# Performance work log

Measured on AMD Instinct MI355X. Metric: run time of the kernel, lower is better.

## Reference

```python
import jax, jax.numpy as jnp
import numpy as np

V, E, T, H, NT, B = 30000, 300, 256, 256, 9, 128


def setup_inputs() -> dict:
    key = jax.random.key(0)
    ks = jax.random.split(key, 12)
    s = 0.05
    # token ids with trailing zero padding (0 = pad), lens in [T//2, T]
    lens = jax.random.randint(ks[0], (B,), T // 2, T + 1)
    tokens = jax.random.randint(ks[1], (B, T), 1, V)
    pos = jnp.arange(T)[None, :]
    inputs = jnp.where(pos < lens[:, None], tokens, 0)
    labels = jax.random.randint(ks[2], (B, T), 0, NT)
    emb = jax.random.normal(ks[3], (V, E), jnp.float32) * s
    Wf = jax.random.normal(ks[4], (E, 4 * H), jnp.float32) * s
    Uf = jax.random.normal(ks[5], (H, 4 * H), jnp.float32) * s
    bf = jnp.zeros((4 * H,), jnp.float32)
    Wb = jax.random.normal(ks[6], (E, 4 * H), jnp.float32) * s
    Ub = jax.random.normal(ks[7], (H, 4 * H), jnp.float32) * s
    bb = jnp.zeros((4 * H,), jnp.float32)
    fcW = jax.random.normal(ks[8], (2 * H, NT), jnp.float32) * s
    fcb = jnp.zeros((NT,), jnp.float32)
    trans = jax.random.uniform(ks[9], (NT, NT), jnp.float32)  # tf.random.uniform init
    return dict(inputs=inputs, labels=labels, emb=emb, Wf=Wf, Uf=Uf, bf=bf,
                Wb=Wb, Ub=Ub, bb=bb, fcW=fcW, fcb=fcb, trans=trans)


def _lstm(x, W, U, b):
    """Keras LSTM (gate order i,f,g,o). x: [B,T,E] -> [B,T,H]."""
    xW = jnp.einsum('bte,eh->bth', x, W) + b  # precompute input projections

    def step(carry, xt):
        h, c = carry
        z = xt + h @ U
        i, f, g, o = jnp.split(z, 4, axis=-1)
        i = jax.nn.sigmoid(i)
        f = jax.nn.sigmoid(f)
        g = jnp.tanh(g)
        o = jax.nn.sigmoid(o)
        c = f * c + i * g
        h = o * jnp.tanh(c)
        return (h, c), h

    Bq = x.shape[0]
    Hq = U.shape[0]
    init = (jnp.zeros((Bq, Hq), x.dtype), jnp.zeros((Bq, Hq), x.dtype))
    _, hs = jax.lax.scan(step, init, jnp.swapaxes(xW, 0, 1))  # [T,B,H]
    return jnp.swapaxes(hs, 0, 1)


def _crf_log_likelihood(logits, labels, lens, trans):
    """tfa.text.crf_log_likelihood: gold score - log partition. logits: [B,T,N]."""
    Bq, Tq, Nq = logits.shape
    pos = jnp.arange(Tq)[None, :]
    mask = pos < lens[:, None]  # [B,T]
    # unary (emission) score of the gold path
    unary = jnp.take_along_axis(logits, labels[..., None], axis=-1)[..., 0]
    score = jnp.sum(jnp.where(mask, unary, 0.0), axis=-1)
    # binary (transition) score of the gold path
    btrans = trans[labels[:, :-1], labels[:, 1:]]
    bmask = pos[:, 1:] < lens[:, None]
    score = score + jnp.sum(jnp.where(bmask, btrans, 0.0), axis=-1)
    # forward algorithm (log partition) with per-timestep length masking
    def step(alpha, inp):
        logit_t, m_t = inp  # [B,N], [B]
        new = jax.nn.logsumexp(alpha[:, :, None] + trans[None], axis=1) + logit_t
        return jnp.where(m_t[:, None], new, alpha), None

    alpha0 = logits[:, 0]
    xs = (jnp.swapaxes(logits[:, 1:], 0, 1), jnp.swapaxes(mask[:, 1:], 0, 1))
    alpha, _ = jax.lax.scan(step, alpha0, xs)
    log_norm = jax.nn.logsumexp(alpha, axis=-1)
    return score - log_norm


def reference(inputs, labels, emb, Wf, Uf, bf, Wb, Ub, bb, fcW, fcb, trans):
    text_lens = jnp.sum((inputs != 0).astype(jnp.int32), axis=-1)
    x = emb[inputs]  # [B,T,E]
    hf = _lstm(x, Wf, Uf, bf)
    hb = _lstm(x[:, ::-1], Wb, Ub, bb)[:, ::-1]
    h = jnp.concatenate([hf, hb], axis=-1)  # [B,T,2H]
    logits = h @ fcW + fcb  # [B,T,NT]
    log_likelihood = _crf_log_likelihood(logits, labels, text_lens, trans)
    return logits, log_likelihood, text_lens
```

## Files before the change

kernel.cpp:

```cpp
#include <hip/hip_runtime.h>
#include <hip/hip_bf16.h>
#include <stdint.h>

#define Bb 128
#define Tt 256
#define Ee 300
#define EP 320
#define Hh 256
#define G4 1024
#define NTAG 9

typedef __bf16 bf16x8 __attribute__((ext_vector_type(8)));
typedef float f32x4 __attribute__((ext_vector_type(4)));
typedef float f32x2 __attribute__((ext_vector_type(2)));
typedef int i32x8 __attribute__((ext_vector_type(8)));
typedef unsigned short u16;
typedef unsigned int u32;
typedef unsigned char u8;
typedef long i64;

union U4B { uint4 q; bf16x8 v; };

static __device__ __forceinline__ float bf2f(u32 u){
  union { float f; u32 u; } w; w.u = u << 16; return w.f;
}
static __device__ __forceinline__ u16 f2bf(float f){
  union { float f; u32 u; } w; w.f = f;
  u32 x = w.u;
  return (u16)((x + 0x7fffu + ((x >> 16) & 1u)) >> 16);
}
static __device__ __forceinline__ int perm2orig(int c){
  int w = c >> 7, r = c & 127, g = r >> 5, jj = r & 31;
  return g * 256 + w * 32 + jj;
}
static __device__ __forceinline__ float frcp(float x){ return __builtin_amdgcn_rcpf(x); }
static __device__ __forceinline__ float fexp2(float x){
  float r; asm("v_exp_f32 %0, %1" : "=v"(r) : "v"(x)); return r;
}
static __device__ __forceinline__ f32x2 vexp2(f32x2 x){
  f32x2 r; r[0] = fexp2(x[0]); r[1] = fexp2(x[1]); return r;
}
static __device__ __forceinline__ f32x2 vrcp(f32x2 x){
  f32x2 r; r[0] = frcp(x[0]); r[1] = frcp(x[1]); return r;
}
static __device__ __forceinline__ f32x2 vfabs(f32x2 x){
  f32x2 r; r[0] = __builtin_fabsf(x[0]); r[1] = __builtin_fabsf(x[1]); return r;
}
static __device__ __forceinline__ f32x2 vminc(f32x2 x, float c){
  f32x2 r; r[0] = fminf(x[0], c); r[1] = fminf(x[1], c); return r;
}
static __device__ __forceinline__ f32x2 vcps(f32x2 m, f32x2 s){
  f32x2 r; r[0] = __builtin_copysignf(m[0], s[0]);
  r[1] = __builtin_copysignf(m[1], s[1]); return r;
}
static __device__ __forceinline__ void gl_lds16(const void* g, void* l){
  __builtin_amdgcn_global_load_lds((const __attribute__((address_space(1))) u32*)(g),
                                   (__attribute__((address_space(3))) u32*)(l), 16, 0, 0);
}

__global__ void prep_k(const float* __restrict__ Wf, const float* __restrict__ Wb,
                       const float* __restrict__ Uf, const float* __restrict__ Ub,
                       const float* __restrict__ bf_, const float* __restrict__ bb_,
                       const float* __restrict__ fcW,
                       u16* __restrict__ Wpk, u8* __restrict__ Upk8,
                       float* __restrict__ bperm, u8* __restrict__ fcw8){
  int blk = blockIdx.x;
  if(blk < 320){
    int idx = blk * 256 + threadIdx.x;
    if(idx >= 128 * 10 * 64) return;
    int lane = idx & 63;
    int kk = (idx >> 6) % 10;
    int nt2 = idx / 640;
    int d = nt2 >> 6, ntd = nt2 & 63;
    int oc = perm2orig(ntd * 16 + (lane & 15));
    const float* W = d ? Wb : Wf;
    int k0 = kk * 32 + ((lane >> 4) << 3);
    u16 o[8];
    #pragma unroll
    for(int j = 0; j < 8; ++j){
      int k = k0 + j;
      o[j] = (k < Ee) ? f2bf(W[(size_t)k * G4 + oc]) : (u16)0;
    }
    uint4 q;
    q.x = o[0] | ((u32)o[1] << 16); q.y = o[2] | ((u32)o[3] << 16);
    q.z = o[4] | ((u32)o[5] << 16); q.w = o[6] | ((u32)o[7] << 16);
    *(uint4*)(Wpk + (size_t)idx * 8) = q;
  } else if(blk < 384){
    int idx = (blk - 320) * 256 + threadIdx.x;
    if(idx >= 2 * 64 * 2 * 64) return;
    int lane = idx & 63;
    int kh = (idx >> 6) & 1;
    int nt = (idx >> 7) & 63;
    int d = idx >> 13;
    int oc = perm2orig(nt * 16 + (lane & 15));
    const float* U = d ? Ub : Uf;
    int k0 = kh * 128 + (lane >> 4) * 32;
    u32 o[8];
    #pragma unroll
    for(int m = 0; m < 8; ++m){
      float v0 = U[(size_t)(k0 + 4 * m + 0) * G4 + oc] * 32.f;
      float v1 = U[(size_t)(k0 + 4 * m + 1) * G4 + oc] * 32.f;
      float v2 = U[(size_t)(k0 + 4 * m + 2) * G4 + oc] * 32.f;
      float v3 = U[(size_t)(k0 + 4 * m + 3) * G4 + oc] * 32.f;
      int pk = __builtin_amdgcn_cvt_pk_fp8_f32(v0, v1, 0, false);
      pk = __builtin_amdgcn_cvt_pk_fp8_f32(v2, v3, pk, true);
      o[m] = (u32)pk;
    }
    uint4* dst = (uint4*)(Upk8 + (size_t)idx * 32);
    dst[0] = (uint4){o[0], o[1], o[2], o[3]};
    dst[1] = (uint4){o[4], o[5], o[6], o[7]};
  } else if(blk < 392){
    int c = (blk - 384) * 256 + threadIdx.x;
    if(c >= 2048) return;
    const float* src = (c >> 10) ? bb_ : bf_;
    bperm[c] = src[perm2orig(c & 1023)];
  } else {
    int idx = (blk - 392) * 256 + threadIdx.x;
    if(idx >= 1024) return;
    int lane = idx & 63, kk = idx >> 6;
    int col = lane & 15;
    int k0 = kk * 32 + ((lane >> 4) << 3);
    float v[8];
    #pragma unroll
    for(int j = 0; j < 8; ++j)
      v[j] = (col < NTAG) ? fcW[(size_t)(k0 + j) * NTAG + col] * 256.f : 0.f;
    int lo = __builtin_amdgcn_cvt_pk_fp8_f32(v[0], v[1], 0, false);
    lo = __builtin_amdgcn_cvt_pk_fp8_f32(v[2], v[3], lo, true);
    int hi = __builtin_amdgcn_cvt_pk_fp8_f32(v[4], v[5], 0, false);
    hi = __builtin_amdgcn_cvt_pk_fp8_f32(v[6], v[7], hi, true);
    uint2 q; q.x = (u32)lo; q.y = (u32)hi;
    *(uint2*)(fcw8 + (size_t)idx * 8) = q;
  }
}

__global__ void gather_x_k(const int* __restrict__ inp, const float* __restrict__ emb,
                           u16* __restrict__ xbf){
  int row = blockIdx.x * 2 + (threadIdx.x >> 7);
  int j = threadIdx.x & 127;
  int t = row >> 7, b = row & 127;
  int tok = inp[b * Tt + t];
  u16* dst = xbf + (size_t)row * EP;
  if(j < 75){
    float4 v = *(const float4*)(emb + (size_t)tok * Ee + j * 4);
    u32 lo = f2bf(v.x) | ((u32)f2bf(v.y) << 16);
    u32 hi = f2bf(v.z) | ((u32)f2bf(v.w) << 16);
    *(uint2*)(dst + j * 4) = (uint2){lo, hi};
  } else if(j < 80){
    *(uint2*)(dst + j * 4) = (uint2){0u, 0u};
  }
}

__global__ __launch_bounds__(256, 2) void xw_gemm_k(const u16* __restrict__ xbf,
    const u16* __restrict__ Wpk, const float* __restrict__ bperm,
    u16* __restrict__ xwpk){
  __shared__ uint4 At[2][512];
  int t0 = blockIdx.y * 2, nblk = blockIdx.x;
  int tid = threadIdx.x, lane = tid & 63, w = tid >> 6;
  int mh = w >> 1, nh = w & 1;
  f32x4 acc[2][4][4];
  #pragma unroll
  for(int tt = 0; tt < 2; ++tt)
    #pragma unroll
    for(int i = 0; i < 4; ++i)
      #pragma unroll
      for(int j = 0; j < 4; ++j) acc[tt][i][j] = (f32x4){0.f, 0.f, 0.f, 0.f};
  for(int ks = 0; ks < 10; ++ks){
    __syncthreads();
    #pragma unroll
    for(int it = 0; it < 2; ++it){
      int row = it * 64 + w * 16 + (lane >> 2);
      int seg = (lane & 3) ^ (row & 3);
      gl_lds16(xbf + (size_t)(t0 * 128 + row) * EP + ks * 32 + seg * 8,
               &At[0][it * 256 + w * 64]);
      gl_lds16(xbf + (size_t)((t0 + 1) * 128 + row) * EP + ks * 32 + seg * 8,
               &At[1][it * 256 + w * 64]);
    }
    asm volatile("s_waitcnt vmcnt(0)" ::: "memory");
    __syncthreads();
    U4B bv[4];
    #pragma unroll
    for(int n = 0; n < 4; ++n){
      int ntg = nblk * 8 + nh * 4 + n;
      bv[n].q = *(const uint4*)(Wpk + ((size_t)(ntg * 10 + ks) * 64 + lane) * 8);
    }
    #pragma unroll
    for(int tt = 0; tt < 2; ++tt){
      U4B a[4];
      #pragma unroll
      for(int m = 0; m < 4; ++m){
        int row = (mh * 4 + m) * 16 + (lane & 15);
        a[m].q = At[tt][row * 4 + ((lane >> 4) ^ (row & 3))];
      }
      #pragma unroll
      for(int m = 0; m < 4; ++m)
        #pragma unroll
        for(int n = 0; n < 4; ++n)
          acc[tt][m][n] = __builtin_amdgcn_mfma_f32_16x16x32_bf16(a[m].v, bv[n].v, acc[tt][m][n], 0, 0, 0);
    }
  }
  #pragma unroll
  for(int tt = 0; tt < 2; ++tt){
    int t = t0 + tt;
    #pragma unroll
    for(int m = 0; m < 4; ++m){
      int grp = mh * 4 + m;
      #pragma unroll
      for(int n = 0; n < 4; ++n){
        int ntg = nblk * 8 + nh * 4 + n;
        int d = ntg >> 6, nd = ntg & 63;
        float bias = bperm[ntg * 16 + (lane & 15)];
        u16 h0 = f2bf((acc[tt][m][n][0] + bias) * 512.f), h1 = f2bf((acc[tt][m][n][1] + bias) * 512.f);
        u16 h2 = f2bf((acc[tt][m][n][2] + bias) * 512.f), h3 = f2bf((acc[tt][m][n][3] + bias) * 512.f);
        uint2 p; p.x = h0 | ((u32)h1 << 16); p.y = h2 | ((u32)h3 << 16);
        *(uint2*)(xwpk + ((((size_t)(d * 8 + grp) * Tt + t) * 64 + nd) * 64 + lane) * 4) = p;
      }
    }
  }
}

__global__ __launch_bounds__(512, 2) void lstm_rec_k(const u16* __restrict__ xwpk,
    const u8* __restrict__ Upk8, u8* __restrict__ hseq8){
  __shared__ u32 Hf8[2][1024];
  __shared__ uint2 Xw[2][4096];
  int bid = blockIdx.x;
  int d = bid >> 3, grp = bid & 7;
  int tid = threadIdx.x, lane = tid & 63, w = tid >> 6;
  int arow = lane & 15, r4 = lane >> 4;

  i32x8 Ureg[8][2];
  const u8* Ub8 = Upk8 + (size_t)d * 262144;
  #pragma unroll
  for(int n = 0; n < 8; ++n)
    #pragma unroll
    for(int kh = 0; kh < 2; ++kh)
      Ureg[n][kh] = *(const i32x8*)(Ub8 + (((size_t)(w * 8 + n) * 2 + kh) * 64 + lane) * 32);
  #pragma unroll
  for(int n = 0; n < 8; ++n)
    #pragma unroll
    for(int kh = 0; kh < 2; ++kh)
      asm volatile("" : "+a"(Ureg[n][kh]));

  Hf8[0][tid] = 0u; Hf8[0][tid + 512] = 0u;
  f32x2 cst2[2][2];
  #pragma unroll
  for(int a = 0; a < 2; ++a)
    #pragma unroll
    for(int p = 0; p < 2; ++p) cst2[a][p] = (f32x2){0.f, 0.f};
  const u16* xwb = xwpk + (size_t)(d * 8 + grp) * Tt * 16384;
  u8* hs_base = hseq8 + (size_t)(d * 8 + grp) * Tt * 4096;
  u32 hf8base = (u32)(uintptr_t)(&Hf8[0][0]);
  u32* hf8u = (u32*)(&Hf8[0][0]);

  const float c1s = -1.44269504f / 512.f;
  const f32x2 C1  = (f32x2){c1s, c1s};
  const f32x2 C2  = (f32x2){2.f * c1s, 2.f * c1s};
  const f32x2 C3  = (f32x2){-2.f * 1.44269504f, -2.f * 1.44269504f};
  const f32x2 ONE = (f32x2){1.f, 1.f};

  {
    int t0 = d ? (Tt - 1) : 0;
    const u16* xwt0 = xwb + (size_t)t0 * 16384;
    #pragma unroll
    for(int j = 0; j < 4; ++j)
      gl_lds16(xwt0 + (w * 8 + 2 * j) * 256 + lane * 8, &Xw[0][w * 512 + 2 * j * 64]);
  }
  asm volatile("s_waitcnt vmcnt(0)" ::: "memory");
  __syncthreads();

  int cur = 0;
  for(int st = 0; st < Tt; ++st){
    int t = d ? (Tt - 1 - st) : st;
    int p = st & 1, c_ = p ^ 1;
    union AFU { i64 dd[4]; i32x8 v; };
    AFU af0, af1;
    u32 av = hf8base + (u32)(p * 4096) + (u32)(r4 * 512 + arow * 8);
    asm volatile("ds_read_b64_tr_b8 %0, %1"             : "=v"(af0.dd[0]) : "v"(av));
    asm volatile("ds_read_b64_tr_b8 %0, %1 offset:128"  : "=v"(af0.dd[1]) : "v"(av));
    asm volatile("ds_read_b64_tr_b8 %0, %1 offset:256"  : "=v"(af0.dd[2]) : "v"(av));
    asm volatile("ds_read_b64_tr_b8 %0, %1 offset:384"  : "=v"(af0.dd[3]) : "v"(av));
    asm volatile("ds_read_b64_tr_b8 %0, %1 offset:2048" : "=v"(af1.dd[0]) : "v"(av));
    asm volatile("ds_read_b64_tr_b8 %0, %1 offset:2176" : "=v"(af1.dd[1]) : "v"(av));
    asm volatile("ds_read_b64_tr_b8 %0, %1 offset:2304" : "=v"(af1.dd[2]) : "v"(av));
    asm volatile("ds_read_b64_tr_b8 %0, %1 offset:2432" : "=v"(af1.dd[3]) : "v"(av));
    asm volatile("s_waitcnt lgkmcnt(0)" ::: "memory");
    __builtin_amdgcn_sched_barrier(0);
    asm volatile("s_waitcnt vmcnt(2)" ::: "memory");
    uint2 xw[8];
    #pragma unroll
    for(int n = 0; n < 8; ++n) xw[n] = Xw[cur][w * 512 + n * 64 + lane];
    {
      int stn = (st + 1 < Tt) ? st + 1 : st;
      int tn = d ? (Tt - 1 - stn) : stn;
      const u16* xwtn = xwb + (size_t)tn * 16384;
      #pragma unroll
      for(int j = 0; j < 4; ++j)
        gl_lds16(xwtn + (w * 8 + 2 * j) * 256 + lane * 8, &Xw[cur ^ 1][w * 512 + 2 * j * 64]);
    }
    __builtin_amdgcn_sched_barrier(0);
    f32x4 acc[8];
    #pragma unroll
    for(int n = 0; n < 8; ++n){
      acc[n][0] = bf2f(xw[n].x & 0xffffu);
      acc[n][1] = bf2f(xw[n].x >> 16);
      acc[n][2] = bf2f(xw[n].y & 0xffffu);
      acc[n][3] = bf2f(xw[n].y >> 16);
    }
    #pragma unroll
    for(int n = 0; n < 8; ++n){
      asm volatile("v_mfma_f32_16x16x128_f8f6f4 %0, %1, %2, %0"
                   : "+v"(acc[n]) : "v"(af0.v), "a"(Ureg[n][0]));
      asm volatile("v_mfma_f32_16x16x128_f8f6f4 %0, %1, %2, %0"
                   : "+v"(acc[n]) : "v"(af1.v), "a"(Ureg[n][1]));
    }
    #pragma unroll
    for(int n1 = 0; n1 < 2; ++n1){
      f32x2 h16[2];
      #pragma unroll
      for(int pq = 0; pq < 2; ++pq){
        f32x2 ai = (f32x2){acc[0 + n1][2 * pq], acc[0 + n1][2 * pq + 1]};
        f32x2 af = (f32x2){acc[2 + n1][2 * pq], acc[2 + n1][2 * pq + 1]};
        f32x2 ag = (f32x2){acc[4 + n1][2 * pq], acc[4 + n1][2 * pq + 1]};
        f32x2 ao = (f32x2){acc[6 + n1][2 * pq], acc[6 + n1][2 * pq + 1]};
        f32x2 ei = vexp2(ai * C1);
        f32x2 ef = vexp2(af * C1);
        f32x2 eo = vexp2(ao * C1);
        f32x2 eg = vexp2(vminc(vfabs(ag), 10240.f) * C2);
        f32x2 ig = vcps(ONE - eg, ag) * vrcp((ONE + ei) * (ONE + eg));
        f32x2 fs = vrcp(ONE + ef);
        f32x2 cc = fs * cst2[n1][pq] + ig;
        cst2[n1][pq] = cc;
        f32x2 ec = vexp2(vminc(vfabs(cc), 20.f) * C3);
        f32x2 hh = vcps(ONE - ec, cc) * vrcp((ONE + eo) * (ONE + ec));
        h16[pq] = hh * (f32x2){16.f, 16.f};
      }
      int pk = __builtin_amdgcn_cvt_pk_fp8_f32(h16[0][0], h16[0][1], 0, false);
      pk = __builtin_amdgcn_cvt_pk_fp8_f32(h16[1][0], h16[1][1], pk, true);
      int unit = w * 32 + n1 * 16 + arow;
      hf8u[c_ * 1024 + unit * 4 + r4] = (u32)pk;
      *(u32*)(hs_base + (size_t)t * 4096 + unit * 16 + r4 * 4) = (u32)pk;
    }
    asm volatile("s_waitcnt lgkmcnt(0)" ::: "memory");
    __builtin_amdgcn_s_barrier();
    cur ^= 1;
  }
}

__global__ __launch_bounds__(256) void logits_k(const u8* __restrict__ hseq8,
    const u8* __restrict__ fcw8, const float* __restrict__ fcb,
    float* __restrict__ out){
  __shared__ u8 Ht[4][8192];
  int widx = threadIdx.x >> 6, lane = threadIdx.x & 63;
  int wid = blockIdx.x * 4 + widx;
  int grp = wid >> 8, t = wid & 255;
  i64 bf[16];
  #pragma unroll
  for(int kk = 0; kk < 16; ++kk)
    bf[kk] = *(const i64*)(fcw8 + ((size_t)kk * 64 + lane) * 8);
  const u8* hf = hseq8 + ((size_t)(0 * 8 + grp) * Tt + t) * 4096;
  const u8* hb = hseq8 + ((size_t)(1 * 8 + grp) * Tt + t) * 4096;
  #pragma unroll
  for(int j = 0; j < 4; ++j){
    gl_lds16(hf + j * 1024 + lane * 16, &Ht[widx][j * 1024]);
    gl_lds16(hb + j * 1024 + lane * 16, &Ht[widx][4096 + j * 1024]);
  }
  asm volatile("s_waitcnt vmcnt(0)" ::: "memory");
  __builtin_amdgcn_sched_barrier(0);
  u32 base = (u32)(uintptr_t)(&Ht[widx][0]) + lane * 8;
  i64 afr[16];
  #pragma unroll
  for(int kk = 0; kk < 16; ++kk){
    u32 a = base + kk * 512;
    asm volatile("ds_read_b64_tr_b8 %0, %1" : "=v"(afr[kk]) : "v"(a));
  }
  asm volatile("s_waitcnt lgkmcnt(0)" ::: "memory");
  __builtin_amdgcn_sched_barrier(0);
  f32x4 acc = (f32x4){0.f, 0.f, 0.f, 0.f};
  #pragma unroll
  for(int kk = 0; kk < 16; ++kk)
    acc = __builtin_amdgcn_mfma_f32_16x16x32_fp8_fp8(afr[kk], bf[kk], acc, 0, 0, 0);
  int tag = lane & 15, r4 = lane >> 4;
  if(tag < NTAG){
    float bb = fcb[tag];
    #pragma unroll
    for(int q = 0; q < 4; ++q){
      int b = grp * 16 + r4 * 4 + q;
      out[((size_t)b * Tt + t) * NTAG + tag] = acc[q] * (1.f / 4096.f) + bb;
    }
  }
}

__global__ __launch_bounds__(64) void crf_k(const int* __restrict__ inp,
    const int* __restrict__ labels, const float* __restrict__ trans,
    const float* __restrict__ logits, float* __restrict__ out){
  int b = blockIdx.x;
  int lane = threadIdx.x;
  int cnt = 0;
  for(int t = lane; t < Tt; t += 64) cnt += (inp[b * Tt + t] != 0) ? 1 : 0;
  #pragma unroll
  for(int off = 32; off >= 1; off >>= 1) cnt += __shfl_xor(cnt, off, 64);
  int len = cnt;
  float sc = 0.f;
  for(int t = lane; t < Tt; t += 64){
    if(t < len){
      int lab = labels[b * Tt + t];
      sc += logits[(size_t)(b * Tt + t) * NTAG + lab];
      if(t >= 1){
        int lp = labels[b * Tt + t - 1];
        sc += trans[lp * NTAG + lab];
      }
    }
  }
  #pragma unroll
  for(int off = 32; off >= 1; off >>= 1) sc += __shfl_xor(sc, off, 64);
  float Tc[NTAG];
  if(lane < NTAG){
    #pragma unroll
    for(int i = 0; i < NTAG; ++i) Tc[i] = trans[i * NTAG + lane];
  }
  float alpha = (lane < NTAG) ? logits[(size_t)(b * Tt) * NTAG + lane] : -3.0e38f;
  for(int t = 1; t < len; ++t){
    float av[NTAG];
    #pragma unroll
    for(int i = 0; i < NTAG; ++i) av[i] = __shfl(alpha, i, 64);
    if(lane < NTAG){
      float m = av[0] + Tc[0];
      #pragma unroll
      for(int i = 1; i < NTAG; ++i) m = fmaxf(m, av[i] + Tc[i]);
      float s = 0.f;
      #pragma unroll
      for(int i = 0; i < NTAG; ++i) s += __expf(av[i] + Tc[i] - m);
      alpha = __logf(s) + m + logits[(size_t)(b * Tt + t) * NTAG + lane];
    }
  }
  float av[NTAG];
  #pragma unroll
  for(int i = 0; i < NTAG; ++i) av[i] = __shfl(alpha, i, 64);
  float m = av[0];
  #pragma unroll
  for(int i = 1; i < NTAG; ++i) m = fmaxf(m, av[i]);
  float s = 0.f;
  #pragma unroll
  for(int i = 0; i < NTAG; ++i) s += __expf(av[i] - m);
  float ln = __logf(s) + m;
  if(lane == 0){
    out[(size_t)Bb * Tt * NTAG + b] = sc - ln;
    out[(size_t)Bb * Tt * NTAG + Bb + b] = (float)len;
  }
}

extern "C" void kernel_launch(void* const* d_in, const int* in_sizes, int n_in,
                              void* d_out, int out_size, void* d_ws, size_t ws_size,
                              hipStream_t stream) {
  const int*   inputs = (const int*)d_in[0];
  const int*   labels = (const int*)d_in[1];
  const float* emb    = (const float*)d_in[2];
  const float* Wf     = (const float*)d_in[3];
  const float* Uf     = (const float*)d_in[4];
  const float* bf_    = (const float*)d_in[5];
  const float* Wb     = (const float*)d_in[6];
  const float* Ub     = (const float*)d_in[7];
  const float* bb_    = (const float*)d_in[8];
  const float* fcW    = (const float*)d_in[9];
  const float* fcb    = (const float*)d_in[10];
  const float* trans  = (const float*)d_in[11];
  float* out = (float*)d_out;
  char* ws = (char*)d_ws;
  u16*   xwpk  = (u16*)(ws + 0);
  u8*    hseq8 = (u8*) (ws + 134217728);
  u8*    Upk8  = (u8*) (ws + 150994944);
  u16*   Wpk   = (u16*)(ws + 151519232);
  float* bperm = (float*)(ws + 152829952);
  u8*    fcw8  = (u8*) (ws + 152838144);
  u16*   xbf   = (u16*)(ws + 152846336);

  hipLaunchKernelGGL(prep_k, dim3(396), dim3(256), 0, stream,
                     Wf, Wb, Uf, Ub, bf_, bb_, fcW, Wpk, Upk8, bperm, fcw8);
  hipLaunchKernelGGL(gather_x_k, dim3(16384), dim3(256), 0, stream, inputs, emb, xbf);
  hipLaunchKernelGGL(xw_gemm_k, dim3(16, 128), dim3(256), 0, stream, xbf, Wpk, bperm, xwpk);
  hipLaunchKernelGGL(lstm_rec_k, dim3(16), dim3(512), 0, stream, xwpk, Upk8, hseq8);
  hipLaunchKernelGGL(logits_k, dim3(512), dim3(256), 0, stream, hseq8, fcw8, fcb, out);
  hipLaunchKernelGGL(crf_k, dim3(128), dim3(64), 0, stream, inputs, labels, trans, out, out);
}
```

Measured before the change: 580.0 us.

## Prefetch recurrent input projections into registers and merge gather into prep kernel

```diff
diff --git a/kernel.cpp b/kernel.cpp
--- a/kernel.cpp
+++ b/kernel.cpp
@@ -61,9 +61,11 @@
 __global__ void prep_k(const float* __restrict__ Wf, const float* __restrict__ Wb,
                        const float* __restrict__ Uf, const float* __restrict__ Ub,
                        const float* __restrict__ bf_, const float* __restrict__ bb_,
-                       const float* __restrict__ fcW,
+                       const float* __restrict__ fcW, const int* __restrict__ inp,
+                       const float* __restrict__ emb,
                        u16* __restrict__ Wpk, u8* __restrict__ Upk8,
-                       float* __restrict__ bperm, u8* __restrict__ fcw8){
+                       float* __restrict__ bperm, u8* __restrict__ fcw8,
+                       u16* __restrict__ xbf){
   int blk = blockIdx.x;
   if(blk < 320){
     int idx = blk * 256 + threadIdx.x;
@@ -114,7 +116,7 @@
     if(c >= 2048) return;
     const float* src = (c >> 10) ? bb_ : bf_;
     bperm[c] = src[perm2orig(c & 1023)];
-  } else {
+  } else if(blk < 396){
     int idx = (blk - 392) * 256 + threadIdx.x;
     if(idx >= 1024) return;
     int lane = idx & 63, kk = idx >> 6;
@@ -130,23 +132,20 @@
     hi = __builtin_amdgcn_cvt_pk_fp8_f32(v[6], v[7], hi, true);
     uint2 q; q.x = (u32)lo; q.y = (u32)hi;
     *(uint2*)(fcw8 + (size_t)idx * 8) = q;
-  }
-}
-
-__global__ void gather_x_k(const int* __restrict__ inp, const float* __restrict__ emb,
-                           u16* __restrict__ xbf){
-  int row = blockIdx.x * 2 + (threadIdx.x >> 7);
-  int j = threadIdx.x & 127;
-  int t = row >> 7, b = row & 127;
-  int tok = inp[b * Tt + t];
-  u16* dst = xbf + (size_t)row * EP;
-  if(j < 75){
-    float4 v = *(const float4*)(emb + (size_t)tok * Ee + j * 4);
-    u32 lo = f2bf(v.x) | ((u32)f2bf(v.y) << 16);
-    u32 hi = f2bf(v.z) | ((u32)f2bf(v.w) << 16);
-    *(uint2*)(dst + j * 4) = (uint2){lo, hi};
-  } else if(j < 80){
-    *(uint2*)(dst + j * 4) = (uint2){0u, 0u};
+  } else {
+    int row = (blk - 396) * 2 + (threadIdx.x >> 7);
+    int j = threadIdx.x & 127;
+    int t = row >> 7, b = row & 127;
+    int tok = inp[b * Tt + t];
+    u16* dst = xbf + (size_t)row * EP;
+    if(j < 75){
+      float4 v = *(const float4*)(emb + (size_t)tok * Ee + j * 4);
+      u32 lo = f2bf(v.x) | ((u32)f2bf(v.y) << 16);
+      u32 hi = f2bf(v.z) | ((u32)f2bf(v.w) << 16);
+      *(uint2*)(dst + j * 4) = (uint2){lo, hi};
+    } else if(j < 80){
+      *(uint2*)(dst + j * 4) = (uint2){0u, 0u};
+    }
   }
 }
 
@@ -221,7 +220,6 @@
 __global__ __launch_bounds__(512, 2) void lstm_rec_k(const u16* __restrict__ xwpk,
     const u8* __restrict__ Upk8, u8* __restrict__ hseq8){
   __shared__ u32 Hf8[2][1024];
-  __shared__ uint2 Xw[2][4096];
   int bid = blockIdx.x;
   int d = bid >> 3, grp = bid & 7;
   int tid = threadIdx.x, lane = tid & 63, w = tid >> 6;
@@ -257,18 +255,17 @@
   const f32x2 C3  = (f32x2){-2.f * 1.44269504f, -2.f * 1.44269504f};
   const f32x2 ONE = (f32x2){1.f, 1.f};
 
+  uint2 xva[8], xvb[8];
   {
     int t0 = d ? (Tt - 1) : 0;
     const u16* xwt0 = xwb + (size_t)t0 * 16384;
     #pragma unroll
-    for(int j = 0; j < 4; ++j)
-      gl_lds16(xwt0 + (w * 8 + 2 * j) * 256 + lane * 8, &Xw[0][w * 512 + 2 * j * 64]);
-  }
-  asm volatile("s_waitcnt vmcnt(0)" ::: "memory");
+    for(int n = 0; n < 8; ++n)
+      xva[n] = *(const uint2*)(xwt0 + ((size_t)(w * 8 + n) * 64 + lane) * 4);
+  }
   __syncthreads();
 
-  int cur = 0;
-  for(int st = 0; st < Tt; ++st){
+  auto STEP = [&](int st, uint2* xvin, uint2* xvout){
     int t = d ? (Tt - 1 - st) : st;
     int p = st & 1, c_ = p ^ 1;
     union AFU { i64 dd[4]; i32x8 v; };
@@ -284,27 +281,23 @@
     asm volatile("ds_read_b64_tr_b8 %0, %1 offset:2432" : "=v"(af1.dd[3]) : "v"(av));
     asm volatile("s_waitcnt lgkmcnt(0)" ::: "memory");
     __builtin_amdgcn_sched_barrier(0);
-    asm volatile("s_waitcnt vmcnt(2)" ::: "memory");
-    uint2 xw[8];
-    #pragma unroll
-    for(int n = 0; n < 8; ++n) xw[n] = Xw[cur][w * 512 + n * 64 + lane];
+    f32x4 acc[8];
+    #pragma unroll
+    for(int n = 0; n < 8; ++n){
+      acc[n][0] = bf2f(xvin[n].x & 0xffffu);
+      acc[n][1] = bf2f(xvin[n].x >> 16);
+      acc[n][2] = bf2f(xvin[n].y & 0xffffu);
+      acc[n][3] = bf2f(xvin[n].y >> 16);
+    }
     {
       int stn = (st + 1 < Tt) ? st + 1 : st;
       int tn = d ? (Tt - 1 - stn) : stn;
       const u16* xwtn = xwb + (size_t)tn * 16384;
       #pragma unroll
-      for(int j = 0; j < 4; ++j)
-        gl_lds16(xwtn + (w * 8 + 2 * j) * 256 + lane * 8, &Xw[cur ^ 1][w * 512 + 2 * j * 64]);
+      for(int n = 0; n < 8; ++n)
+        xvout[n] = *(const uint2*)(xwtn + ((size_t)(w * 8 + n) * 64 + lane) * 4);
     }
     __builtin_amdgcn_sched_barrier(0);
-    f32x4 acc[8];
-    #pragma unroll
-    for(int n = 0; n < 8; ++n){
-      acc[n][0] = bf2f(xw[n].x & 0xffffu);
-      acc[n][1] = bf2f(xw[n].x >> 16);
-      acc[n][2] = bf2f(xw[n].y & 0xffffu);
-      acc[n][3] = bf2f(xw[n].y >> 16);
-    }
     #pragma unroll
     for(int n = 0; n < 8; ++n){
       asm volatile("v_mfma_f32_16x16x128_f8f6f4 %0, %1, %2, %0"
@@ -341,7 +334,11 @@
     }
     asm volatile("s_waitcnt lgkmcnt(0)" ::: "memory");
     __builtin_amdgcn_s_barrier();
-    cur ^= 1;
+  };
+
+  for(int st = 0; st < Tt; st += 2){
+    STEP(st, xva, xvb);
+    STEP(st + 1, xvb, xva);
   }
 }
 
@@ -473,9 +470,9 @@
   u8*    fcw8  = (u8*) (ws + 152838144);
   u16*   xbf   = (u16*)(ws + 152846336);
 
-  hipLaunchKernelGGL(prep_k, dim3(396), dim3(256), 0, stream,
-                     Wf, Wb, Uf, Ub, bf_, bb_, fcW, Wpk, Upk8, bperm, fcw8);
-  hipLaunchKernelGGL(gather_x_k, dim3(16384), dim3(256), 0, stream, inputs, emb, xbf);
+  hipLaunchKernelGGL(prep_k, dim3(396 + 16384), dim3(256), 0, stream,
+                     Wf, Wb, Uf, Ub, bf_, bb_, fcW, inputs, emb,
+                     Wpk, Upk8, bperm, fcw8, xbf);
   hipLaunchKernelGGL(xw_gemm_k, dim3(16, 128), dim3(256), 0, stream, xbf, Wpk, bperm, xwpk);
   hipLaunchKernelGGL(lstm_rec_k, dim3(16), dim3(512), 0, stream, xwpk, Upk8, hseq8);
   hipLaunchKernelGGL(logits_k, dim3(512), dim3(256), 0, stream, hseq8, fcw8, fcb, out);
```

New measurement: 594.6 us. +2.5%, slower.
